# Kernel tuning notes

Hardware: AMD Instinct MI355X
Metric: run time of the kernel (lower is better)

Reference implementation:

```python
import jax, jax.numpy as jnp
import numpy as np

N = 50000
E_RAND = 800000
IN_CH = 128
HID = 64
HEADS = 4
OUT_CH = 3
NEG_SLOPE = 0.2
BN_EPS = 1e-5


def setup_inputs() -> dict:
    key = jax.random.key(0)
    ks = jax.random.split(key, 24)
    x = jax.random.normal(ks[0], (N, IN_CH), dtype=jnp.float32)
    er = jax.random.randint(ks[1], (2, E_RAND), 0, N)
    sl = jnp.tile(jnp.arange(N, dtype=er.dtype)[None, :], (2, 1))
    edge_index = jnp.concatenate([er, sl], axis=1)  # [2, 850000]
    s = 0.1
    d1 = HID * HEADS            # 256
    d2 = (HID // 2) * HEADS     # 128
    inp = dict(x=x, edge_index=edge_index)
    # layer 1: in 128 -> heads*64
    inp["W1"] = s * jax.random.normal(ks[2], (IN_CH, HEADS * HID), dtype=jnp.float32)
    inp["a1s"] = s * jax.random.normal(ks[3], (HEADS, HID), dtype=jnp.float32)
    inp["a1d"] = s * jax.random.normal(ks[4], (HEADS, HID), dtype=jnp.float32)
    inp["b1"] = jnp.zeros((d1,), jnp.float32)
    inp["g1"] = jnp.ones((d1,), jnp.float32)
    inp["be1"] = jnp.zeros((d1,), jnp.float32)
    inp["m1"] = 0.01 * jax.random.normal(ks[5], (d1,), dtype=jnp.float32)
    inp["v1"] = jnp.ones((d1,), jnp.float32) + 0.01 * jax.random.uniform(ks[6], (d1,))
    # layer 2: in 256 -> heads*32
    inp["W2"] = s * jax.random.normal(ks[7], (d1, HEADS * (HID // 2)), dtype=jnp.float32)
    inp["a2s"] = s * jax.random.normal(ks[8], (HEADS, HID // 2), dtype=jnp.float32)
    inp["a2d"] = s * jax.random.normal(ks[9], (HEADS, HID // 2), dtype=jnp.float32)
    inp["b2"] = jnp.zeros((d2,), jnp.float32)
    inp["g2"] = jnp.ones((d2,), jnp.float32)
    inp["be2"] = jnp.zeros((d2,), jnp.float32)
    inp["m2"] = 0.01 * jax.random.normal(ks[10], (d2,), dtype=jnp.float32)
    inp["v2"] = jnp.ones((d2,), jnp.float32) + 0.01 * jax.random.uniform(ks[11], (d2,))
    # layer 3: in 128 -> 1 head, out_ch, concat=False
    inp["W3"] = s * jax.random.normal(ks[12], (d2, OUT_CH), dtype=jnp.float32)
    inp["a3s"] = s * jax.random.normal(ks[13], (1, OUT_CH), dtype=jnp.float32)
    inp["a3d"] = s * jax.random.normal(ks[14], (1, OUT_CH), dtype=jnp.float32)
    inp["b3"] = jnp.zeros((OUT_CH,), jnp.float32)
    return inp


def gat_conv(x, src, dst, W, a_src, a_dst, b, heads, fdim, concat):
    n = x.shape[0]
    h = (x @ W).reshape(n, heads, fdim)           # [N,H,F]
    als = jnp.einsum('nhf,hf->nh', h, a_src)      # [N,H]
    ald = jnp.einsum('nhf,hf->nh', h, a_dst)
    e = jax.nn.leaky_relu(als[src] + ald[dst], NEG_SLOPE)  # [E,H]
    m = jax.lax.stop_gradient(jax.ops.segment_max(e, dst, num_segments=n))
    ex = jnp.exp(e - m[dst])
    ssum = jax.ops.segment_sum(ex, dst, num_segments=n)
    alpha = ex / (ssum[dst] + 1e-16)              # segment softmax over in-edges
    msg = h[src] * alpha[:, :, None]              # [E,H,F]
    out = jax.ops.segment_sum(msg, dst, num_segments=n)  # [N,H,F]
    out = out.reshape(n, heads * fdim) if concat else out.mean(axis=1)
    return out + b


def batch_norm(x, gamma, beta, mean, var):
    return (x - mean) * jax.lax.rsqrt(var + BN_EPS) * gamma + beta


def reference(x, edge_index, W1, a1s, a1d, b1, g1, be1, m1, v1,
              W2, a2s, a2d, b2, g2, be2, m2, v2,
              W3, a3s, a3d, b3):
    src, dst = edge_index[0], edge_index[1]
    h = gat_conv(x, src, dst, W1, a1s, a1d, b1, HEADS, HID, True)
    h = jax.nn.elu(batch_norm(h, g1, be1, m1, v1))
    h = gat_conv(h, src, dst, W2, a2s, a2d, b2, HEADS, HID // 2, True)
    h = jax.nn.elu(batch_norm(h, g2, be2, m2, v2))
    h = gat_conv(h, src, dst, W3, a3s, a3d, b3, 1, OUT_CH, False)
    return jax.nn.log_softmax(h, axis=1)
```

## Files before the change

kernel.cpp:

```cpp
#include <hip/hip_runtime.h>


#define WSZ 64

typedef short short8 __attribute__((ext_vector_type(8)));
typedef short short4v __attribute__((ext_vector_type(4)));
typedef float float4v __attribute__((ext_vector_type(4)));
typedef float f2v __attribute__((ext_vector_type(2)));
typedef unsigned uint2v __attribute__((ext_vector_type(2)));

__device__ inline unsigned short f2bf(float f) {
  unsigned u = __float_as_uint(f);
  u += 0x7FFFu + ((u >> 16) & 1u);
  return (unsigned short)(u >> 16);
}
__device__ inline float bf2f(unsigned short u) {
  return __uint_as_float(((unsigned)u) << 16);
}


__global__ __launch_bounds__(256) void hist_kernel(const int* __restrict__ dst, int E,
                                                   int* __restrict__ deg) {
  int e = blockIdx.x * 256 + threadIdx.x;
  if (e < E) atomicAdd(&deg[dst[e]], 1);
}

__global__ __launch_bounds__(256) void block_sums_kernel(const int* __restrict__ deg, int n,
                                                         int* __restrict__ bsum) {
  __shared__ int sh[256];
  int t = threadIdx.x;
  int base = blockIdx.x * 1024 + t * 4;
  int v = 0;
#pragma unroll
  for (int j = 0; j < 4; ++j) {
    int idx = base + j;
    if (idx < n) v += deg[idx];
  }
  sh[t] = v;
  __syncthreads();
  for (int off = 128; off >= 1; off >>= 1) {
    if (t < off) sh[t] += sh[t + off];
    __syncthreads();
  }
  if (t == 0) bsum[blockIdx.x] = sh[0];
}

__global__ void tiny_scan_kernel(int* bsum, int nb) {
  if (threadIdx.x == 0 && blockIdx.x == 0) {
    int run = 0;
    for (int i = 0; i < nb; ++i) {
      int v = bsum[i];
      bsum[i] = run;
      run += v;
    }
  }
}

__global__ __launch_bounds__(256) void scan_write_kernel(const int* __restrict__ deg, int n,
                                                         const int* __restrict__ bbase,
                                                         int* __restrict__ row_start,
                                                         int* __restrict__ cursor) {
  __shared__ int sh[256];
  int t = threadIdx.x;
  int base = blockIdx.x * 1024 + t * 4;
  int v[4];
  int s = 0;
#pragma unroll
  for (int j = 0; j < 4; ++j) {
    int idx = base + j;
    v[j] = (idx < n) ? deg[idx] : 0;
    s += v[j];
  }
  sh[t] = s;
  __syncthreads();
  for (int off = 1; off < 256; off <<= 1) {
    int x = (t >= off) ? sh[t - off] : 0;
    __syncthreads();
    sh[t] += x;
    __syncthreads();
  }
  int excl = sh[t] - s + bbase[blockIdx.x];
#pragma unroll
  for (int j = 0; j < 4; ++j) {
    int idx = base + j;
    if (idx < n) {
      row_start[idx] = excl;
      cursor[idx] = excl;
    }
    excl += v[j];
  }
  if (blockIdx.x == gridDim.x - 1 && t == 255) row_start[n] = excl;
}

__global__ __launch_bounds__(256) void scatter_kernel(const int* __restrict__ src,
                                                      const int* __restrict__ dst, int E,
                                                      int* __restrict__ cursor,
                                                      int* __restrict__ csr_src) {
  int e = blockIdx.x * 256 + threadIdx.x;
  if (e < E) {
    int d = dst[e];
    int p = atomicAdd(&cursor[d], 1);
    csr_src[p] = src[e];
  }
}


__global__ __launch_bounds__(256) void conv_w1t_kernel(const float* __restrict__ W1,
                                                       unsigned short* __restrict__ W1t) {
  int idx = blockIdx.x * 256 + threadIdx.x;
  int n = idx >> 7, k = idx & 127;
  W1t[idx] = f2bf(W1[k * 256 + n]);
}

__global__ __launch_bounds__(256) void conv_w2t_kernel(const float* __restrict__ W2,
                                                       unsigned short* __restrict__ W2t) {
  int idx = blockIdx.x * 256 + threadIdx.x;
  int n = idx >> 8, p = idx & 255;
  int kl = (p & ~63) | ((p & 3) << 4) | ((p >> 2) & 15);
  W2t[idx] = f2bf(W2[kl * 128 + n]);
}

__global__ __launch_bounds__(512) void bn_prep_kernel(
    const float* __restrict__ b1, const float* __restrict__ g1,
    const float* __restrict__ be1, const float* __restrict__ m1,
    const float* __restrict__ v1, const float* __restrict__ b2,
    const float* __restrict__ g2, const float* __restrict__ be2,
    const float* __restrict__ m2, const float* __restrict__ v2,
    float* __restrict__ sc1, float* __restrict__ sh1,
    float* __restrict__ sc2, float* __restrict__ sh2) {
  int t = threadIdx.x;
  if (t < 256) {
    float s = g1[t] * rsqrtf(v1[t] + 1e-5f);
    sc1[t] = s;
    sh1[t] = (b1[t] - m1[t]) * s + be1[t];
  } else if (t < 384) {
    int i = t - 256;
    float s = g2[i] * rsqrtf(v2[i] + 1e-5f);
    sc2[i] = s;
    sh2[i] = (b2[i] - m2[i]) * s + be2[i];
  }
}


template <int K, int BN, bool AF32>
__global__ __launch_bounds__(256) void gemm_mfma(
    const void* __restrict__ Ap,
    const unsigned short* __restrict__ Bt,
    const float* __restrict__ a_s, const float* __restrict__ a_d,
    unsigned short* __restrict__ hout,
    float* __restrict__ als, float* __restrict__ ald,
    int M) {
  constexpr int CF = BN / 64;
  constexpr int SF = BN / 8;
  constexpr int PAD = 36;
  __shared__ unsigned short As[64][PAD];
  __shared__ unsigned short Bs[BN][PAD];
  const int t = threadIdx.x;
  const int w = t >> 6;
  const int lane = t & 63;
  const int c16 = lane & 15;
  const int q = lane >> 4;
  const int bm = blockIdx.x * 64;
  const int arow = t >> 2;
  const int akc = (t & 3) * 8;

  float4v acc[4][CF];
#pragma unroll
  for (int rf = 0; rf < 4; ++rf)
#pragma unroll
    for (int cf = 0; cf < CF; ++cf) acc[rf][cf] = float4v{0.f, 0.f, 0.f, 0.f};

  for (int k0 = 0; k0 < K; k0 += 32) {
    {
      int gr = bm + arow;
      if constexpr (AF32) {
        const float* Af = (const float*)Ap + (size_t)gr * K + k0 + akc;
        float4 v0 = make_float4(0.f, 0.f, 0.f, 0.f), v1 = v0;
        if (gr < M) {
          v0 = *(const float4*)Af;
          v1 = *(const float4*)(Af + 4);
        }
        ushort4 u0, u1;
        u0.x = f2bf(v0.x); u0.y = f2bf(v0.y); u0.z = f2bf(v0.z); u0.w = f2bf(v0.w);
        u1.x = f2bf(v1.x); u1.y = f2bf(v1.y); u1.z = f2bf(v1.z); u1.w = f2bf(v1.w);
        *(ushort4*)&As[arow][akc] = u0;
        *(ushort4*)&As[arow][akc + 4] = u1;
      } else {
        uint4 v = make_uint4(0u, 0u, 0u, 0u);
        if (gr < M) v = *(const uint4*)((const unsigned short*)Ap + (size_t)gr * K + k0 + akc);
        *(uint2*)&As[arow][akc] = make_uint2(v.x, v.y);
        *(uint2*)&As[arow][akc + 4] = make_uint2(v.z, v.w);
      }
    }
#pragma unroll
    for (int h = 0; h < BN / 64; ++h) {
      int n = (t >> 2) + h * 64;
      uint4 v = *(const uint4*)(Bt + (size_t)n * K + k0 + akc);
      *(uint2*)&Bs[n][akc] = make_uint2(v.x, v.y);
      *(uint2*)&Bs[n][akc + 4] = make_uint2(v.z, v.w);
    }
    __syncthreads();
    short8 af[4], bfr[CF];
#pragma unroll
    for (int rf = 0; rf < 4; ++rf) {
      short4v lo = *(short4v*)&As[rf * 16 + c16][q * 8];
      short4v hi = *(short4v*)&As[rf * 16 + c16][q * 8 + 4];
      af[rf] = __builtin_shufflevector(lo, hi, 0, 1, 2, 3, 4, 5, 6, 7);
    }
#pragma unroll
    for (int cf = 0; cf < CF; ++cf) {
      int n = w * (CF * 16) + cf * 16 + c16;
      short4v lo = *(short4v*)&Bs[n][q * 8];
      short4v hi = *(short4v*)&Bs[n][q * 8 + 4];
      bfr[cf] = __builtin_shufflevector(lo, hi, 0, 1, 2, 3, 4, 5, 6, 7);
    }
#pragma unroll
    for (int rf = 0; rf < 4; ++rf)
#pragma unroll
      for (int cf = 0; cf < CF; ++cf)
        acc[rf][cf] =
            __builtin_amdgcn_mfma_f32_16x16x32_bf16(af[rf], bfr[cf], acc[rf][cf], 0, 0, 0);
    __syncthreads();
  }

  float sasv[CF], sadv[CF];
#pragma unroll
  for (int cf = 0; cf < CF; ++cf) {
    int L = w * (CF * 16) + cf * 16 + c16;
    sasv[cf] = a_s[L];
    sadv[cf] = a_d[L];
  }
  const size_t sub = (size_t)(w * 2 + (c16 >> 3)) * (size_t)M * SF;
#pragma unroll
  for (int rf = 0; rf < 4; ++rf) {
#pragma unroll
    for (int r = 0; r < 4; ++r) {
      int n = bm + rf * 16 + q * 4 + r;
      float ps = 0.f, pd = 0.f;
      unsigned short us[CF];
#pragma unroll
      for (int cf = 0; cf < CF; ++cf) {
        float v = acc[rf][cf][r];
        us[cf] = f2bf(v);
        ps += v * sasv[cf];
        pd += v * sadv[cf];
      }
#pragma unroll
      for (int off = 1; off <= 8; off <<= 1) {
        ps += __shfl_xor(ps, off, 16);
        pd += __shfl_xor(pd, off, 16);
      }
      if (n < M) {
        if constexpr (CF == 4) {
          ushort4 u;
          u.x = us[0]; u.y = us[1]; u.z = us[2]; u.w = us[3];
          *(ushort4*)(hout + sub + (size_t)n * 32 + (c16 & 7) * 4) = u;
        } else {
          ushort2 u;
          u.x = us[0]; u.y = us[1];
          *(ushort2*)(hout + sub + (size_t)n * 16 + (c16 & 7) * 2) = u;
        }
        if (c16 == 0) {
          als[(size_t)n * 4 + w] = ps;
          ald[(size_t)n * 4 + w] = pd;
        }
      }
    }
  }
}


template <int D>
__global__ __launch_bounds__(256) void gat_agg_slice(
    const unsigned short* __restrict__ h_sl,
    const float* __restrict__ als, const float* __restrict__ ald,
    const int* __restrict__ row_start, const int* __restrict__ csr_src,
    const float* __restrict__ bnsc, const float* __restrict__ bnsh,
    unsigned short* __restrict__ obf,
    float* __restrict__ of32,
    int n_nodes) {
  constexpr int SFEAT = D / 8;
  constexpr int KF = SFEAT / 8;
  constexpr int CAP = 1280;
  __shared__ int s_s[CAP];
  __shared__ float s_a[CAP];
  const int sl = blockIdx.x & 7;
  const int g = blockIdx.x >> 3;
  const int tid = threadIdx.x;
  const int wid = tid >> 6, lane = tid & 63;
  const int f = lane & 7;
  const int ng = lane >> 3;
  const int head = sl >> 1;
  const char* hb = (const char*)(h_sl + (size_t)sl * (unsigned)n_nodes * SFEAT);
  const unsigned uoff = (unsigned)(f * KF * 2);

  const int nb0 = g * 32;
  int rs = __builtin_amdgcn_readfirstlane(row_start[nb0]);
  int re = __builtin_amdgcn_readfirstlane(row_start[min(nb0 + 32, n_nodes)]);
  const bool fast = (re - rs) <= CAP;
  if (fast) {
    for (int i = rs + tid; i < re; i += 256) {
      int s = csr_src[i];
      s_s[i - rs] = s;
      s_a[i - rs] = als[(size_t)(unsigned)s * 4 + head];
    }
  }
  __syncthreads();

  const int lb = (D == 256 ? head * 64 : head * 32) + (sl & 1) * 8 + f;
  float sc0 = bnsc[lb], sh0v = bnsh[lb];
  float sc1 = bnsc[lb + 16], sh1v = bnsh[lb + 16];
  float sc2 = 0.f, sh2v = 0.f, sc3 = 0.f, sh3v = 0.f;
  if constexpr (D == 256) {
    sc2 = bnsc[lb + 32]; sh2v = bnsh[lb + 32];
    sc3 = bnsc[lb + 48]; sh3v = bnsh[lb + 48];
  }

  int n = nb0 + wid * 8 + ng;
  bool valid = n < n_nodes;
  int row = valid ? row_start[n] : rs;
  int deg = valid ? (row_start[n + 1] - row) : 0;
  float aldv = ald[(size_t)(unsigned)(valid ? n : 0) * 4 + head];
  int mx = deg;
#pragma unroll
  for (int off = 8; off <= 32; off <<= 1) mx = max(mx, __shfl_xor(mx, off, 64));
  mx = __builtin_amdgcn_readfirstlane(mx);

  float acc0 = 0.f, acc1 = 0.f, acc2 = 0.f, acc3 = 0.f, ssum = 0.f;

#define AGG_BODY(SGET, AGET)                                        \
  {                                                                 \
    bool act = j < deg;                                             \
    int jo = act ? j : 0;                                           \
    int s = (SGET);                                                 \
    float av = (AGET);                                              \
    float e = av + aldv;                                            \
    e = fmaxf(e, 0.2f * e);                                         \
    float ex = __expf(e);                                           \
    ex = act ? ex : 0.f;                                            \
    ssum += ex;                                                     \
    if constexpr (D == 256) {                                       \
      uint2v u = *(const uint2v*)(hb + ((unsigned)s * 64u + uoff)); \
      acc0 += ex * __uint_as_float(u.x << 16);                      \
      acc1 += ex * __uint_as_float(u.x & 0xffff0000u);              \
      acc2 += ex * __uint_as_float(u.y << 16);                      \
      acc3 += ex * __uint_as_float(u.y & 0xffff0000u);              \
    } else {                                                        \
      unsigned u = *(const unsigned*)(hb + ((unsigned)s * 32u + uoff)); \
      acc0 += ex * __uint_as_float(u << 16);                        \
      acc1 += ex * __uint_as_float(u & 0xffff0000u);                \
    }                                                               \
  }

  if (fast) {
    int base = row - rs;
#pragma unroll 4
    for (int j = 0; j < mx; ++j) AGG_BODY(s_s[base + jo], s_a[base + jo])
  } else {
#pragma unroll 2
    for (int j = 0; j < mx; ++j)
      AGG_BODY(csr_src[row + jo], als[(size_t)(unsigned)s * 4 + head])
  }
#undef AGG_BODY

  if (valid) {
    float inv = 1.f / (ssum + 1e-16f);
    if constexpr (D == 256) {
      float o0 = acc0 * inv, o1 = acc1 * inv, o2 = acc2 * inv, o3 = acc3 * inv;
      float v0 = o0 * sc0 + sh0v;
      float v1 = o1 * sc1 + sh1v;
      float v2 = o2 * sc2 + sh2v;
      float v3 = o3 * sc3 + sh3v;
      v0 = (v0 > 0.f) ? v0 : (__expf(v0) - 1.f);
      v1 = (v1 > 0.f) ? v1 : (__expf(v1) - 1.f);
      v2 = (v2 > 0.f) ? v2 : (__expf(v2) - 1.f);
      v3 = (v3 > 0.f) ? v3 : (__expf(v3) - 1.f);
      uint2v pk;
      pk.x = (unsigned)f2bf(v0) | ((unsigned)f2bf(v1) << 16);
      pk.y = (unsigned)f2bf(v2) | ((unsigned)f2bf(v3) << 16);
      __builtin_nontemporal_store(
          pk, (uint2v*)(obf + (size_t)n * 256 + sl * 32 + f * 4));
    } else {
      float o0 = acc0 * inv, o1 = acc1 * inv;
      float v0 = o0 * sc0 + sh0v;
      float v1 = o1 * sc1 + sh1v;
      v0 = (v0 > 0.f) ? v0 : (__expf(v0) - 1.f);
      v1 = (v1 > 0.f) ? v1 : (__expf(v1) - 1.f);
      f2v v2;
      v2.x = v0; v2.y = v1;
      __builtin_nontemporal_store(
          v2, (f2v*)(of32 + (size_t)n * 128 + sl * 16 + f * 2));
    }
  }
}


__global__ __launch_bounds__(256) void l3_prep_kernel(
    const float* __restrict__ o2, const float* __restrict__ W3,
    const float* __restrict__ a3s, const float* __restrict__ a3d,
    float4* __restrict__ h3p, float* __restrict__ ald3, int n_nodes) {
  __shared__ float w3s[384];
  __shared__ float sa3[6];
  for (int i = threadIdx.x; i < 384; i += 256) w3s[i] = W3[i];
  if (threadIdx.x < 3) {
    sa3[threadIdx.x] = a3s[threadIdx.x];
    sa3[3 + threadIdx.x] = a3d[threadIdx.x];
  }
  __syncthreads();
  int wid = threadIdx.x >> 6, lane = threadIdx.x & 63;
  int n = blockIdx.x * 4 + wid;
  if (n >= n_nodes) return;
  f2v v = *(const f2v*)(o2 + (size_t)n * 128 + lane * 2);
  int hd = lane >> 4;
  int k0l = hd * 32 + (lane & 15);
  int k1l = k0l + 16;
  float p0 = v.x * w3s[k0l * 3 + 0] + v.y * w3s[k1l * 3 + 0];
  float p1 = v.x * w3s[k0l * 3 + 1] + v.y * w3s[k1l * 3 + 1];
  float p2 = v.x * w3s[k0l * 3 + 2] + v.y * w3s[k1l * 3 + 2];
#pragma unroll
  for (int off = 32; off >= 1; off >>= 1) {
    p0 += __shfl_xor(p0, off, 64);
    p1 += __shfl_xor(p1, off, 64);
    p2 += __shfl_xor(p2, off, 64);
  }
  if (lane == 0) {
    float als3 = p0 * sa3[0] + p1 * sa3[1] + p2 * sa3[2];
    float ad3 = p0 * sa3[3] + p1 * sa3[4] + p2 * sa3[5];
    h3p[n] = make_float4(p0, p1, p2, als3);
    ald3[n] = ad3;
  }
}


__global__ __launch_bounds__(256) void l3_agg_kernel(const float4* __restrict__ h3p,
                                                     const float* __restrict__ ald3,
                                                     const int* __restrict__ row_start,
                                                     const int* __restrict__ csr_src,
                                                     const float* __restrict__ b3,
                                                     float* __restrict__ out, int n_nodes) {
  int wid = threadIdx.x >> 6, lane = threadIdx.x & 63;
  int n = __builtin_amdgcn_readfirstlane(blockIdx.x * 4 + wid);
  if (n >= n_nodes) return;
  float aldv = ald3[n];
  int row = __builtin_amdgcn_readfirstlane(row_start[n]);
  int end = __builtin_amdgcn_readfirstlane(row_start[n + 1]);
  const char* hp = (const char*)h3p;
  float a0 = 0.f, a1 = 0.f, a2 = 0.f, ss = 0.f;
  for (int i = row + lane; i < end; i += 64) {
    int s = csr_src[i];
    float4 hv = *(const float4*)(hp + ((unsigned)s * 16u));
    float e = hv.w + aldv;
    e = fmaxf(e, 0.2f * e);
    float ex = __expf(e);
    ss += ex;
    a0 += ex * hv.x;
    a1 += ex * hv.y;
    a2 += ex * hv.z;
  }
#pragma unroll
  for (int off = 32; off >= 1; off >>= 1) {
    a0 += __shfl_xor(a0, off, 64);
    a1 += __shfl_xor(a1, off, 64);
    a2 += __shfl_xor(a2, off, 64);
    ss += __shfl_xor(ss, off, 64);
  }
  if (lane == 0) {
    float inv = 1.f / (ss + 1e-16f);
    float o0 = a0 * inv + b3[0];
    float o1 = a1 * inv + b3[1];
    float o2 = a2 * inv + b3[2];
    float m = fmaxf(o0, fmaxf(o1, o2));
    float lse = m + logf(expf(o0 - m) + expf(o1 - m) + expf(o2 - m));
    out[n * 3 + 0] = o0 - lse;
    out[n * 3 + 1] = o1 - lse;
    out[n * 3 + 2] = o2 - lse;
  }
}


extern "C" void kernel_launch(void* const* d_in, const int* in_sizes, int n_in,
                              void* d_out, int out_size, void* d_ws, size_t ws_size,
                              hipStream_t stream) {
  const float* x   = (const float*)d_in[0];
  const int*   ei  = (const int*)d_in[1];
  const float* W1  = (const float*)d_in[2];
  const float* a1s = (const float*)d_in[3];
  const float* a1d = (const float*)d_in[4];
  const float* b1  = (const float*)d_in[5];
  const float* g1v = (const float*)d_in[6];
  const float* be1 = (const float*)d_in[7];
  const float* m1  = (const float*)d_in[8];
  const float* v1  = (const float*)d_in[9];
  const float* W2  = (const float*)d_in[10];
  const float* a2s = (const float*)d_in[11];
  const float* a2d = (const float*)d_in[12];
  const float* b2  = (const float*)d_in[13];
  const float* g2v = (const float*)d_in[14];
  const float* be2 = (const float*)d_in[15];
  const float* m2  = (const float*)d_in[16];
  const float* v2  = (const float*)d_in[17];
  const float* W3  = (const float*)d_in[18];
  const float* a3s = (const float*)d_in[19];
  const float* a3d = (const float*)d_in[20];
  const float* b3  = (const float*)d_in[21];
  float* out = (float*)d_out;

  const int N = in_sizes[0] / 128;
  const int E = in_sizes[1] / 2;
  const int* srcv = ei;
  const int* dstv = ei + E;

  const int eb = (E + 255) / 256;
  const int nb = (N + 1023) / 1024;
  const int nodes4 = (N + 3) / 4;
  const int mblocks = (N + 63) / 64;
  const int aggblocks = ((N + 31) / 32) * 8;

  float* wsf  = (float*)d_ws;
  float* als1 = wsf;
  float* ald1 = als1 + (size_t)N * 4;
  float* als2 = ald1 + (size_t)N * 4;
  float* ald2 = als2 + (size_t)N * 4;
  float* h3p  = ald2 + (size_t)N * 4;
  float* ald3 = h3p + (size_t)N * 4;
  unsigned short* h1s   = (unsigned short*)(ald3 + N);
  unsigned short* o1_bf = h1s + (size_t)N * 256;
  unsigned short* W1t   = o1_bf + (size_t)N * 256;
  unsigned short* W2t   = W1t + 256 * 128;
  int* deg       = (int*)(W2t + 128 * 256);
  int* row_start = deg + N;
  int* cursor    = row_start + (N + 1);
  int* csr_src   = cursor + (N + 1);
  int* bsum      = csr_src + E;
  float* bnsc1 = (float*)(bsum + 1024);
  float* bnsh1 = bnsc1 + 256;
  float* bnsc2 = bnsh1 + 256;
  float* bnsh2 = bnsc2 + 128;
  unsigned short* h2s = (unsigned short*)(bnsh2 + 128);
  float* o2f = (float*)h1s;

  conv_w1t_kernel<<<128, 256, 0, stream>>>(W1, W1t);
  conv_w2t_kernel<<<128, 256, 0, stream>>>(W2, W2t);
  bn_prep_kernel<<<1, 512, 0, stream>>>(b1, g1v, be1, m1, v1, b2, g2v, be2, m2, v2,
                                        bnsc1, bnsh1, bnsc2, bnsh2);

  hipMemsetAsync(deg, 0, (size_t)N * sizeof(int), stream);
  hist_kernel<<<eb, 256, 0, stream>>>(dstv, E, deg);
  block_sums_kernel<<<nb, 256, 0, stream>>>(deg, N, bsum);
  tiny_scan_kernel<<<1, 64, 0, stream>>>(bsum, nb);
  scan_write_kernel<<<nb, 256, 0, stream>>>(deg, N, bsum, row_start, cursor);
  scatter_kernel<<<eb, 256, 0, stream>>>(srcv, dstv, E, cursor, csr_src);

  gemm_mfma<128, 256, true><<<mblocks, 256, 0, stream>>>(x, W1t, a1s, a1d, h1s, als1,
                                                         ald1, N);
  gat_agg_slice<256><<<aggblocks, 256, 0, stream>>>(
      h1s, als1, ald1, row_start, csr_src, bnsc1, bnsh1, o1_bf, nullptr, N);
  gemm_mfma<256, 128, false><<<mblocks, 256, 0, stream>>>(o1_bf, W2t, a2s, a2d, h2s, als2,
                                                          ald2, N);
  gat_agg_slice<128><<<aggblocks, 256, 0, stream>>>(
      h2s, als2, ald2, row_start, csr_src, bnsc2, bnsh2, nullptr, o2f, N);
  l3_prep_kernel<<<nodes4, 256, 0, stream>>>(o2f, W3, a3s, a3d, (float4*)h3p, ald3, N);
  l3_agg_kernel<<<nodes4, 256, 0, stream>>>((const float4*)h3p, ald3, row_start, csr_src,
                                            b3, out, N);
}
```

Baseline: 428.0 us.

## Precompute edge exponentials in LDS and widen layer-2 aggregation gathers

After: 424.2 us. About the same (-0.9%).

```diff
diff --git a/kernel.cpp b/kernel.cpp
--- a/kernel.cpp
+++ b/kernel.cpp
@@ -7,6 +7,7 @@
 typedef short short4v __attribute__((ext_vector_type(4)));
 typedef float float4v __attribute__((ext_vector_type(4)));
 typedef float f2v __attribute__((ext_vector_type(2)));
+typedef float f4v __attribute__((ext_vector_type(4)));
 typedef unsigned uint2v __attribute__((ext_vector_type(2)));
 
 __device__ inline unsigned short f2bf(float f) {
@@ -279,117 +280,133 @@
     unsigned short* __restrict__ obf,
     float* __restrict__ of32,
     int n_nodes) {
-  constexpr int SFEAT = D / 8;
-  constexpr int KF = SFEAT / 8;
   constexpr int CAP = 1280;
   __shared__ int s_s[CAP];
   __shared__ float s_a[CAP];
-  const int sl = blockIdx.x & 7;
+  __shared__ int rb[33];
+  const int slot = blockIdx.x & 7;
   const int g = blockIdx.x >> 3;
   const int tid = threadIdx.x;
   const int wid = tid >> 6, lane = tid & 63;
   const int f = lane & 7;
   const int ng = lane >> 3;
-  const int head = sl >> 1;
-  const char* hb = (const char*)(h_sl + (size_t)sl * (unsigned)n_nodes * SFEAT);
-  const unsigned uoff = (unsigned)(f * KF * 2);
-
-  const int nb0 = g * 32;
-  int rs = __builtin_amdgcn_readfirstlane(row_start[nb0]);
-  int re = __builtin_amdgcn_readfirstlane(row_start[min(nb0 + 32, n_nodes)]);
+  const int hd = (D == 256) ? (slot >> 1) : (slot >> 1);
+  const int nb0 = (D == 256) ? (g * 32) : (g * 64 + (slot & 1) * 32);
+
+  const unsigned short* hbl;
+  if constexpr (D == 256) {
+    hbl = h_sl + (size_t)slot * (size_t)(unsigned)n_nodes * 32 + f * 4;
+  } else {
+    hbl = h_sl + (size_t)(hd * 2 + (f >> 2)) * (size_t)(unsigned)n_nodes * 16 +
+          (f & 3) * 4;
+  }
+
+  if (tid < 33) rb[tid] = row_start[min(nb0 + tid, n_nodes)];
+  __syncthreads();
+  const int rs = __builtin_amdgcn_readfirstlane(rb[0]);
+  const int re = __builtin_amdgcn_readfirstlane(rb[32]);
   const bool fast = (re - rs) <= CAP;
   if (fast) {
     for (int i = rs + tid; i < re; i += 256) {
       int s = csr_src[i];
+      int lo = 0;
+#pragma unroll
+      for (int st = 16; st >= 1; st >>= 1) lo += (i >= rb[lo + st]) ? st : 0;
+      float av = als[(size_t)(unsigned)s * 4 + hd] +
+                 ald[(size_t)(unsigned)(nb0 + lo) * 4 + hd];
+      av = fmaxf(av, 0.2f * av);
       s_s[i - rs] = s;
-      s_a[i - rs] = als[(size_t)(unsigned)s * 4 + head];
+      s_a[i - rs] = __expf(av);
     }
   }
   __syncthreads();
 
-  const int lb = (D == 256 ? head * 64 : head * 32) + (sl & 1) * 8 + f;
-  float sc0 = bnsc[lb], sh0v = bnsh[lb];
-  float sc1 = bnsc[lb + 16], sh1v = bnsh[lb + 16];
-  float sc2 = 0.f, sh2v = 0.f, sc3 = 0.f, sh3v = 0.f;
+  float scv[4], shv[4];
   if constexpr (D == 256) {
-    sc2 = bnsc[lb + 32]; sh2v = bnsh[lb + 32];
-    sc3 = bnsc[lb + 48]; sh3v = bnsh[lb + 48];
+    const int lb = hd * 64 + (slot & 1) * 8 + f;
+#pragma unroll
+    for (int k = 0; k < 4; ++k) {
+      scv[k] = bnsc[lb + k * 16];
+      shv[k] = bnsh[lb + k * 16];
+    }
+  } else {
+#pragma unroll
+    for (int k = 0; k < 4; ++k) {
+      int pin = f * 4 + k;
+      int l = hd * 32 + (pin >> 4) * 8 + ((pin & 15) >> 1) + (pin & 1) * 16;
+      scv[k] = bnsc[l];
+      shv[k] = bnsh[l];
+    }
   }
 
   int n = nb0 + wid * 8 + ng;
   bool valid = n < n_nodes;
   int row = valid ? row_start[n] : rs;
   int deg = valid ? (row_start[n + 1] - row) : 0;
-  float aldv = ald[(size_t)(unsigned)(valid ? n : 0) * 4 + head];
   int mx = deg;
 #pragma unroll
   for (int off = 8; off <= 32; off <<= 1) mx = max(mx, __shfl_xor(mx, off, 64));
   mx = __builtin_amdgcn_readfirstlane(mx);
 
   float acc0 = 0.f, acc1 = 0.f, acc2 = 0.f, acc3 = 0.f, ssum = 0.f;
-
-#define AGG_BODY(SGET, AGET)                                        \
-  {                                                                 \
-    bool act = j < deg;                                             \
-    int jo = act ? j : 0;                                           \
-    int s = (SGET);                                                 \
-    float av = (AGET);                                              \
-    float e = av + aldv;                                            \
-    e = fmaxf(e, 0.2f * e);                                         \
-    float ex = __expf(e);                                           \
-    ex = act ? ex : 0.f;                                            \
-    ssum += ex;                                                     \
-    if constexpr (D == 256) {                                       \
-      uint2v u = *(const uint2v*)(hb + ((unsigned)s * 64u + uoff)); \
-      acc0 += ex * __uint_as_float(u.x << 16);                      \
-      acc1 += ex * __uint_as_float(u.x & 0xffff0000u);              \
-      acc2 += ex * __uint_as_float(u.y << 16);                      \
-      acc3 += ex * __uint_as_float(u.y & 0xffff0000u);              \
-    } else {                                                        \
-      unsigned u = *(const unsigned*)(hb + ((unsigned)s * 32u + uoff)); \
-      acc0 += ex * __uint_as_float(u << 16);                        \
-      acc1 += ex * __uint_as_float(u & 0xffff0000u);                \
-    }                                                               \
-  }
 
   if (fast) {
     int base = row - rs;
 #pragma unroll 4
-    for (int j = 0; j < mx; ++j) AGG_BODY(s_s[base + jo], s_a[base + jo])
+    for (int j = 0; j < mx; ++j) {
+      bool act = j < deg;
+      int idx = base + (act ? j : 0);
+      int s = s_s[idx];
+      float ex = s_a[idx];
+      ex = act ? ex : 0.f;
+      ssum += ex;
+      uint2v u = *(const uint2v*)(hbl + (size_t)(unsigned)s * (D == 256 ? 32 : 16));
+      acc0 += ex * __uint_as_float(u.x << 16);
+      acc1 += ex * __uint_as_float(u.x & 0xffff0000u);
+      acc2 += ex * __uint_as_float(u.y << 16);
+      acc3 += ex * __uint_as_float(u.y & 0xffff0000u);
+    }
   } else {
+    float aldv = ald[(size_t)(unsigned)(valid ? n : 0) * 4 + hd];
 #pragma unroll 2
-    for (int j = 0; j < mx; ++j)
-      AGG_BODY(csr_src[row + jo], als[(size_t)(unsigned)s * 4 + head])
-  }
-#undef AGG_BODY
+    for (int j = 0; j < mx; ++j) {
+      bool act = j < deg;
+      int idx = row + (act ? j : 0);
+      int s = csr_src[idx];
+      float av = als[(size_t)(unsigned)s * 4 + hd] + aldv;
+      av = fmaxf(av, 0.2f * av);
+      float ex = __expf(av);
+      ex = act ? ex : 0.f;
+      ssum += ex;
+      uint2v u = *(const uint2v*)(hbl + (size_t)(unsigned)s * (D == 256 ? 32 : 16));
+      acc0 += ex * __uint_as_float(u.x << 16);
+      acc1 += ex * __uint_as_float(u.x & 0xffff0000u);
+      acc2 += ex * __uint_as_float(u.y << 16);
+      acc3 += ex * __uint_as_float(u.y & 0xffff0000u);
+    }
+  }
 
   if (valid) {
     float inv = 1.f / (ssum + 1e-16f);
+    float v0 = (acc0 * inv) * scv[0] + shv[0];
+    float v1 = (acc1 * inv) * scv[1] + shv[1];
+    float v2 = (acc2 * inv) * scv[2] + shv[2];
+    float v3 = (acc3 * inv) * scv[3] + shv[3];
+    v0 = (v0 > 0.f) ? v0 : (__expf(v0) - 1.f);
+    v1 = (v1 > 0.f) ? v1 : (__expf(v1) - 1.f);
+    v2 = (v2 > 0.f) ? v2 : (__expf(v2) - 1.f);
+    v3 = (v3 > 0.f) ? v3 : (__expf(v3) - 1.f);
     if constexpr (D == 256) {
-      float o0 = acc0 * inv, o1 = acc1 * inv, o2 = acc2 * inv, o3 = acc3 * inv;
-      float v0 = o0 * sc0 + sh0v;
-      float v1 = o1 * sc1 + sh1v;
-      float v2 = o2 * sc2 + sh2v;
-      float v3 = o3 * sc3 + sh3v;
-      v0 = (v0 > 0.f) ? v0 : (__expf(v0) - 1.f);
-      v1 = (v1 > 0.f) ? v1 : (__expf(v1) - 1.f);
-      v2 = (v2 > 0.f) ? v2 : (__expf(v2) - 1.f);
-      v3 = (v3 > 0.f) ? v3 : (__expf(v3) - 1.f);
       uint2v pk;
       pk.x = (unsigned)f2bf(v0) | ((unsigned)f2bf(v1) << 16);
       pk.y = (unsigned)f2bf(v2) | ((unsigned)f2bf(v3) << 16);
       __builtin_nontemporal_store(
-          pk, (uint2v*)(obf + (size_t)n * 256 + sl * 32 + f * 4));
+          pk, (uint2v*)(obf + (size_t)n * 256 + slot * 32 + f * 4));
     } else {
-      float o0 = acc0 * inv, o1 = acc1 * inv;
-      float v0 = o0 * sc0 + sh0v;
-      float v1 = o1 * sc1 + sh1v;
-      v0 = (v0 > 0.f) ? v0 : (__expf(v0) - 1.f);
-      v1 = (v1 > 0.f) ? v1 : (__expf(v1) - 1.f);
-      f2v v2;
-      v2.x = v0; v2.y = v1;
+      f4v v4;
+      v4.x = v0; v4.y = v1; v4.z = v2; v4.w = v3;
       __builtin_nontemporal_store(
-          v2, (f2v*)(of32 + (size_t)n * 128 + sl * 16 + f * 2));
+          v4, (f4v*)(of32 + (size_t)n * 128 + hd * 32 + f * 4));
     }
   }
 }
@@ -514,7 +531,8 @@
   const int nb = (N + 1023) / 1024;
   const int nodes4 = (N + 3) / 4;
   const int mblocks = (N + 63) / 64;
-  const int aggblocks = ((N + 31) / 32) * 8;
+  const int agg1blocks = ((N + 31) / 32) * 8;
+  const int agg2blocks = ((N + 63) / 64) * 8;
 
   float* wsf  = (float*)d_ws;
   float* als1 = wsf;
@@ -553,11 +571,11 @@
 
   gemm_mfma<128, 256, true><<<mblocks, 256, 0, stream>>>(x, W1t, a1s, a1d, h1s, als1,
                                                          ald1, N);
-  gat_agg_slice<256><<<aggblocks, 256, 0, stream>>>(
+  gat_agg_slice<256><<<agg1blocks, 256, 0, stream>>>(
       h1s, als1, ald1, row_start, csr_src, bnsc1, bnsh1, o1_bf, nullptr, N);
   gemm_mfma<256, 128, false><<<mblocks, 256, 0, stream>>>(o1_bf, W2t, a2s, a2d, h2s, als2,
                                                           ald2, N);
-  gat_agg_slice<128><<<aggblocks, 256, 0, stream>>>(
+  gat_agg_slice<128><<<agg2blocks, 256, 0, stream>>>(
       h2s, als2, ald2, row_start, csr_src, bnsc2, bnsh2, nullptr, o2f, N);
   l3_prep_kernel<<<nodes4, 256, 0, stream>>>(o2f, W3, a3s, a3d, (float4*)h3p, ald3, N);
   l3_agg_kernel<<<nodes4, 256, 0, stream>>>((const float4*)h3p, ald3, row_start, csr_src,
```
